# Kernel optimization log

Hardware: AMD Instinct MI355X
Metric: run time of the kernel (lower is better)

The kernel has to match this reference:

```python
import jax, jax.numpy as jnp
import numpy as np

EPS = 1e-5  # F.layer_norm default eps
NEG_SLOPE = 0.01  # nn.LeakyReLU default


def _layer_norm_all(x):
    # F.layer_norm(input, input.size()): normalize over ALL elements, no affine
    m = jnp.mean(x)
    v = jnp.mean(jnp.square(x - m))
    return (x - m) * jax.lax.rsqrt(v + EPS)


def _leaky(x):
    return jnp.where(x >= 0, x, NEG_SLOPE * x)


def setup_inputs() -> dict:
    key = jax.random.key(0)
    ks = jax.random.split(key, 4)
    x = jax.random.normal(ks[0], (10, 10, 4), dtype=jnp.float32)  # HWC observation
    conv_w = jax.random.normal(ks[1], (16, 4, 3, 3), dtype=jnp.float32) * np.sqrt(1.0 / (4 * 3 * 3))
    conv_b = jnp.zeros((16,), dtype=jnp.float32)
    w1 = jax.random.normal(ks[2], (128, 1024), dtype=jnp.float32) * np.sqrt(1.0 / 1024)
    b1 = jnp.zeros((128,), dtype=jnp.float32)
    w2 = jax.random.normal(ks[3], (3, 128), dtype=jnp.float32) * np.sqrt(1.0 / 128)
    b2 = jnp.zeros((3,), dtype=jnp.float32)
    return {"x": x, "conv_w": conv_w, "conv_b": conv_b, "w1": w1, "b1": b1, "w2": w2, "b2": b2}


def reference(x, conv_w, conv_b, w1, b1, w2, b2):
    # x: (H=10, W=10, C=4) -> moveaxis(-1, 0) -> CHW
    h = jnp.moveaxis(x, -1, 0)[None]  # (1, 4, 10, 10)
    h = jax.lax.conv_general_dilated(
        h, conv_w, window_strides=(1, 1), padding='VALID',
        dimension_numbers=('NCHW', 'OIHW', 'NCHW'))[0]  # (16, 8, 8)
    h = h + conv_b[:, None, None]
    h = _leaky(_layer_norm_all(h))
    h = h.reshape(-1)  # (1024,) Flatten(start_dim=0)
    h = w1 @ h + b1  # (128,)
    h = _leaky(_layer_norm_all(h))
    return w2 @ h + b2  # (3,) q-values
```

## Files before the change

### kernel.cpp

```cpp
#include <hip/hip_runtime.h>

#define LN_EPS 1e-5f
#define SLOPE  0.01f

__global__ __launch_bounds__(256) void streamq_k1(
    const float* __restrict__ x,
    const float* __restrict__ cw,
    const float* __restrict__ cb,
    const float* __restrict__ w1,
    const float* __restrict__ b1,
    float* __restrict__ ws_out)
{
    __shared__ float xs[400];
    __shared__ float cws[576];
    __shared__ __align__(16) float hs[1024];
    __shared__ float red1[10];
    __shared__ float red2[4];

    const int tid  = threadIdx.x;
    const int wid  = tid >> 6;
    const int lane = tid & 63;
    const int row  = blockIdx.x;

    const float4* w4 = reinterpret_cast<const float4*>(w1 + (row << 10));
    const float4  wv = w4[tid];

    xs[tid] = x[tid];
    if (tid < 144) xs[tid + 256] = x[tid + 256];
    cws[tid] = cw[tid];
    if (tid < 320) cws[tid + 256] = cw[tid + 256];
    if (tid < 64)  cws[tid + 512] = cw[tid + 512];
    __syncthreads();

    float v[4];
    float s = 0.f, q = 0.f;
    #pragma unroll
    for (int u = 0; u < 4; ++u) {
        const int f = tid + (u << 8);
        const int o = f >> 6, rem = f & 63, i = rem >> 3, j = rem & 7;
        float acc = cb[o];
        const float* wo = &cws[o * 36];
        #pragma unroll
        for (int dh = 0; dh < 3; ++dh)
            #pragma unroll
            for (int dw = 0; dw < 3; ++dw) {
                const float* xp = &xs[((i + dh) * 10 + (j + dw)) * 4];
                #pragma unroll
                for (int c = 0; c < 4; ++c)
                    acc = fmaf(xp[c], wo[c * 9 + dh * 3 + dw], acc);
            }
        v[u] = acc;
        s += acc;
        q += acc * acc;
    }

    #pragma unroll
    for (int off = 32; off; off >>= 1) {
        s += __shfl_down(s, off);
        q += __shfl_down(q, off);
    }
    if (lane == 0) { red1[wid] = s; red1[4 + wid] = q; }
    __syncthreads();
    if (tid == 0) {
        float ss = red1[0] + red1[1] + red1[2] + red1[3];
        float qq = red1[4] + red1[5] + red1[6] + red1[7];
        float m   = ss * (1.0f / 1024.0f);
        float var = qq * (1.0f / 1024.0f) - m * m;
        red1[8] = m;
        red1[9] = rsqrtf(var + LN_EPS);
    }
    __syncthreads();
    {
        const float m = red1[8], r = red1[9];
        #pragma unroll
        for (int u = 0; u < 4; ++u) {
            float hv = (v[u] - m) * r;
            hv = hv >= 0.f ? hv : SLOPE * hv;
            hs[tid + (u << 8)] = hv;
        }
    }
    __syncthreads();

    const float4* h4 = reinterpret_cast<const float4*>(hs);
    const float4  hv = h4[tid];
    float acc = wv.x * hv.x + wv.y * hv.y + wv.z * hv.z + wv.w * hv.w;
    #pragma unroll
    for (int off = 32; off; off >>= 1) acc += __shfl_down(acc, off);
    if (lane == 0) red2[wid] = acc;
    __syncthreads();
    if (tid == 0)
        ws_out[row] = red2[0] + red2[1] + red2[2] + red2[3] + b1[row];
}

__global__ __launch_bounds__(192) void streamq_k2(
    const float* __restrict__ ys_in,
    const float* __restrict__ w2,
    const float* __restrict__ b2,
    float* __restrict__ out)
{
    __shared__ float h2[128];
    __shared__ float red[8];

    const int tid  = threadIdx.x;
    const int wid  = tid >> 6;
    const int lane = tid & 63;

    const float y = (tid < 128) ? ys_in[tid] : 0.f;
    float s = y, q = y * y;
    #pragma unroll
    for (int off = 32; off; off >>= 1) {
        s += __shfl_down(s, off);
        q += __shfl_down(q, off);
    }
    if (lane == 0) { red[wid] = s; red[3 + wid] = q; }
    __syncthreads();
    if (tid == 0) {
        float ss = red[0] + red[1] + red[2];
        float qq = red[3] + red[4] + red[5];
        float m   = ss * (1.0f / 128.0f);
        float var = qq * (1.0f / 128.0f) - m * m;
        red[6] = m;
        red[7] = rsqrtf(var + LN_EPS);
    }
    __syncthreads();
    if (tid < 128) {
        float t = (y - red[6]) * red[7];
        t = t >= 0.f ? t : SLOPE * t;
        h2[tid] = t;
    }
    __syncthreads();

    float acc = w2[wid * 128 + lane] * h2[lane]
              + w2[wid * 128 + 64 + lane] * h2[64 + lane];
    #pragma unroll
    for (int off = 32; off; off >>= 1) acc += __shfl_down(acc, off);
    if (lane == 0) out[wid] = acc + b2[wid];
}

extern "C" void kernel_launch(void* const* d_in, const int* in_sizes, int n_in,
                              void* d_out, int out_size, void* d_ws, size_t ws_size,
                              hipStream_t stream) {
    const float* x  = (const float*)d_in[0];
    const float* cw = (const float*)d_in[1];
    const float* cb = (const float*)d_in[2];
    const float* w1 = (const float*)d_in[3];
    const float* b1 = (const float*)d_in[4];
    const float* w2 = (const float*)d_in[5];
    const float* b2 = (const float*)d_in[6];
    float* out = (float*)d_out;
    float* ys  = (float*)d_ws;

    streamq_k1<<<128, 256, 0, stream>>>(x, cw, cb, w1, b1, ys);
    streamq_k2<<<1, 192, 0, stream>>>(ys, w2, b2, out);
}
```

Before: 11.56 us.

## Fuse both stages into one cooperative kernel with grid sync

The two kernel launches are replaced by a single cooperative launch of 32 blocks. Each wave now computes one output row of the first linear layer, so each block handles four rows instead of one. A grid-wide sync then lets block 0 run the second layernorm and the final linear layer. This removes one kernel launch and cuts the redundant per-block convolution recomputation by a factor of four. In exchange it adds the cost of a grid barrier and of a cooperative launch.

```diff
diff --git a/kernel.cpp b/kernel.cpp
--- a/kernel.cpp
+++ b/kernel.cpp
@@ -1,29 +1,39 @@
 #include <hip/hip_runtime.h>
+#include <hip/hip_cooperative_groups.h>
+
+namespace cg = cooperative_groups;
 
 #define LN_EPS 1e-5f
 #define SLOPE  0.01f
 
-__global__ __launch_bounds__(256) void streamq_k1(
+__global__ __launch_bounds__(256) void streamq_coop(
     const float* __restrict__ x,
     const float* __restrict__ cw,
     const float* __restrict__ cb,
     const float* __restrict__ w1,
     const float* __restrict__ b1,
-    float* __restrict__ ws_out)
+    const float* __restrict__ w2,
+    const float* __restrict__ b2,
+    float* __restrict__ ys,
+    float* __restrict__ out)
 {
     __shared__ float xs[400];
     __shared__ float cws[576];
     __shared__ __align__(16) float hs[1024];
     __shared__ float red1[10];
-    __shared__ float red2[4];
+    __shared__ float h2[128];
+    __shared__ float red2[10];
 
     const int tid  = threadIdx.x;
     const int wid  = tid >> 6;
     const int lane = tid & 63;
-    const int row  = blockIdx.x;
 
+    const int row = (blockIdx.x << 2) | wid;
     const float4* w4 = reinterpret_cast<const float4*>(w1 + (row << 10));
-    const float4  wv = w4[tid];
+    float4 wv0 = w4[lane];
+    float4 wv1 = w4[64 + lane];
+    float4 wv2 = w4[128 + lane];
+    float4 wv3 = w4[192 + lane];
 
     xs[tid] = x[tid];
     if (tid < 144) xs[tid + 256] = x[tid + 256];
@@ -81,60 +91,59 @@
     }
     __syncthreads();
 
-    const float4* h4 = reinterpret_cast<const float4*>(hs);
-    const float4  hv = h4[tid];
-    float acc = wv.x * hv.x + wv.y * hv.y + wv.z * hv.z + wv.w * hv.w;
-    #pragma unroll
-    for (int off = 32; off; off >>= 1) acc += __shfl_down(acc, off);
-    if (lane == 0) red2[wid] = acc;
-    __syncthreads();
-    if (tid == 0)
-        ws_out[row] = red2[0] + red2[1] + red2[2] + red2[3] + b1[row];
-}
+    {
+        const float4* h4 = reinterpret_cast<const float4*>(hs);
+        float4 h0 = h4[lane];
+        float4 h1 = h4[64 + lane];
+        float4 h2v = h4[128 + lane];
+        float4 h3 = h4[192 + lane];
+        float acc = wv0.x * h0.x + wv0.y * h0.y + wv0.z * h0.z + wv0.w * h0.w;
+        acc = fmaf(wv1.x, h1.x, acc); acc = fmaf(wv1.y, h1.y, acc);
+        acc = fmaf(wv1.z, h1.z, acc); acc = fmaf(wv1.w, h1.w, acc);
+        acc = fmaf(wv2.x, h2v.x, acc); acc = fmaf(wv2.y, h2v.y, acc);
+        acc = fmaf(wv2.z, h2v.z, acc); acc = fmaf(wv2.w, h2v.w, acc);
+        acc = fmaf(wv3.x, h3.x, acc); acc = fmaf(wv3.y, h3.y, acc);
+        acc = fmaf(wv3.z, h3.z, acc); acc = fmaf(wv3.w, h3.w, acc);
+        #pragma unroll
+        for (int off = 32; off; off >>= 1) acc += __shfl_down(acc, off);
+        if (lane == 0) ys[row] = acc + b1[row];
+    }
 
-__global__ __launch_bounds__(192) void streamq_k2(
-    const float* __restrict__ ys_in,
-    const float* __restrict__ w2,
-    const float* __restrict__ b2,
-    float* __restrict__ out)
-{
-    __shared__ float h2[128];
-    __shared__ float red[8];
+    cg::this_grid().sync();
 
-    const int tid  = threadIdx.x;
-    const int wid  = tid >> 6;
-    const int lane = tid & 63;
-
-    const float y = (tid < 128) ? ys_in[tid] : 0.f;
-    float s = y, q = y * y;
-    #pragma unroll
-    for (int off = 32; off; off >>= 1) {
-        s += __shfl_down(s, off);
-        q += __shfl_down(q, off);
+    if (blockIdx.x == 0) {
+        const float y = (tid < 128) ? ys[tid] : 0.f;
+        float s2 = y, q2 = y * y;
+        #pragma unroll
+        for (int off = 32; off; off >>= 1) {
+            s2 += __shfl_down(s2, off);
+            q2 += __shfl_down(q2, off);
+        }
+        if (lane == 0) { red2[wid] = s2; red2[4 + wid] = q2; }
+        __syncthreads();
+        if (tid == 0) {
+            float ss = red2[0] + red2[1] + red2[2] + red2[3];
+            float qq = red2[4] + red2[5] + red2[6] + red2[7];
+            float m   = ss * (1.0f / 128.0f);
+            float var = qq * (1.0f / 128.0f) - m * m;
+            red2[8] = m;
+            red2[9] = rsqrtf(var + LN_EPS);
+        }
+        __syncthreads();
+        if (tid < 128) {
+            float t = (y - red2[8]) * red2[9];
+            t = t >= 0.f ? t : SLOPE * t;
+            h2[tid] = t;
+        }
+        __syncthreads();
+        if (wid < 3) {
+            float acc = w2[wid * 128 + lane] * h2[lane]
+                      + w2[wid * 128 + 64 + lane] * h2[64 + lane];
+            #pragma unroll
+            for (int off = 32; off; off >>= 1) acc += __shfl_down(acc, off);
+            if (lane == 0) out[wid] = acc + b2[wid];
+        }
     }
-    if (lane == 0) { red[wid] = s; red[3 + wid] = q; }
-    __syncthreads();
-    if (tid == 0) {
-        float ss = red[0] + red[1] + red[2];
-        float qq = red[3] + red[4] + red[5];
-        float m   = ss * (1.0f / 128.0f);
-        float var = qq * (1.0f / 128.0f) - m * m;
-        red[6] = m;
-        red[7] = rsqrtf(var + LN_EPS);
-    }
-    __syncthreads();
-    if (tid < 128) {
-        float t = (y - red[6]) * red[7];
-        t = t >= 0.f ? t : SLOPE * t;
-        h2[tid] = t;
-    }
-    __syncthreads();
-
-    float acc = w2[wid * 128 + lane] * h2[lane]
-              + w2[wid * 128 + 64 + lane] * h2[64 + lane];
-    #pragma unroll
-    for (int off = 32; off; off >>= 1) acc += __shfl_down(acc, off);
-    if (lane == 0) out[wid] = acc + b2[wid];
 }
 
 extern "C" void kernel_launch(void* const* d_in, const int* in_sizes, int n_in,
@@ -150,6 +159,8 @@
     float* out = (float*)d_out;
     float* ys  = (float*)d_ws;
 
-    streamq_k1<<<128, 256, 0, stream>>>(x, cw, cb, w1, b1, ys);
-    streamq_k2<<<1, 192, 0, stream>>>(ys, w2, b2, out);
+    void* args[] = { (void*)&x, (void*)&cw, (void*)&cb, (void*)&w1, (void*)&b1,
+                     (void*)&w2, (void*)&b2, (void*)&ys, (void*)&out };
+    hipLaunchCooperativeKernel((const void*)streamq_coop, dim3(32), dim3(256),
+                               args, 0, stream);
 }
```

New measurement: 35.58 us. +207.9%, slower.
